# Kernel optimization log

Measured on AMD Instinct MI355X. Metric: run time of the kernel, lower is better.

Reference implementation:

```python
import jax, jax.numpy as jnp
import numpy as np

B, F_C, F_F = 2, 32768, 131072
C_IN, C_OUT, W_DIM, COLOR = 128, 64, 512, 3
K2 = 9
PAD0, PAD1 = 192, 384
ACT_GAIN = float(np.sqrt(2.0))  # lrelu def_gain


def _gather(x, nbr, is_pad, pad):
    # x: [N, C]; nbr: [M, k] indices into [N + pad]; is_pad: [M, k] bool
    padded = jnp.concatenate([x, jnp.zeros((pad, x.shape[1]), x.dtype)], 0)
    g = padded[nbr]  # [M, k, C]
    return jnp.where(is_pad[..., None], jnp.zeros((), x.dtype), g)


def _affine(w, aw, ab):
    # StyleGAN FullyConnectedLayer: runtime weight gain 1/sqrt(fan_in), bias_init=1
    return w @ (aw.T * (1.0 / np.sqrt(aw.shape[1]))) + ab


def _modconv(xg, weight, styles, demodulate=True):
    # xg: [N, k, I]; weight: [O, I, 1, k]; styles: [B, I]
    n, k, ci = xg.shape
    w = weight[:, :, 0, :][None, :, :, :] * styles[:, None, :, None]  # [B,O,I,k]
    if demodulate:
        w = w * jax.lax.rsqrt(jnp.sum(w * w, axis=(2, 3), keepdims=True) + 1e-8)
    xb = xg.reshape(styles.shape[0], -1, k, ci)  # [B,F,k,I]
    return jnp.einsum('bfki,boik->bfo', xb, w).reshape(n, -1)


def _smooth_upsample(x, nbr, is_pad, pad, pool_map):
    # upsample coarse->fine via parent map, then masked neighborhood mean
    xf = x[pool_map]  # [N_fine, C]
    g = _gather(xf, nbr, is_pad, pad)  # [N_fine, k, C]
    cnt = jnp.maximum(jnp.sum(~is_pad, axis=1), 1).astype(x.dtype)
    return jnp.sum(g, axis=1) / cnt[:, None]


def _act(x, gain):
    # clamp_gain(lrelu(x), act_gain*gain, 256*gain)
    y = jnp.where(x >= 0, x, 0.2 * x)
    return jnp.clip(y * (ACT_GAIN * gain), -256.0 * gain, 256.0 * gain)


def setup_inputs():
    key = jax.random.key(0)
    ks = jax.random.split(key, 16)
    x = jax.random.normal(ks[0], (B * F_C, C_IN), jnp.float32)
    img = jax.random.normal(ks[1], (B * F_C, COLOR), jnp.float32)
    ws = jax.random.normal(ks[2], (B, 3, W_DIM), jnp.float32)
    fn0 = jax.random.randint(ks[3], (B * F_C, K2), 0, B * F_C + PAD0, jnp.int32)
    fn1 = jax.random.randint(ks[4], (B * F_F, K2), 0, B * F_F + PAD1, jnp.int32)
    fip0 = jax.random.bernoulli(ks[5], 0.05, (B * F_C, K2))
    fip1 = jax.random.bernoulli(ks[6], 0.05, (B * F_F, K2))
    pool_map0 = jax.random.randint(ks[7], (B * F_F,), 0, B * F_C, jnp.int32)
    a0_w = jax.random.normal(ks[8], (C_IN, W_DIM), jnp.float32)
    a0_b = jnp.ones((C_IN,), jnp.float32)
    W0 = jax.random.normal(ks[9], (C_OUT, C_IN, 1, K2), jnp.float32)
    b0 = jnp.zeros((C_OUT,), jnp.float32)
    ns0 = jnp.zeros((1,), jnp.float32)
    nc0 = jax.random.normal(ks[10], (F_F,), jnp.float32)
    a1_w = jax.random.normal(ks[11], (C_OUT, W_DIM), jnp.float32)
    a1_b = jnp.ones((C_OUT,), jnp.float32)
    W1 = jax.random.normal(ks[12], (C_OUT, C_OUT, 1, K2), jnp.float32)
    b1 = jnp.zeros((C_OUT,), jnp.float32)
    ns1 = jnp.zeros((1,), jnp.float32)
    nc1 = jax.random.normal(ks[13], (F_F,), jnp.float32)
    at_w = jax.random.normal(ks[14], (C_OUT, W_DIM), jnp.float32)
    at_b = jnp.ones((C_OUT,), jnp.float32)
    Wt = jax.random.normal(ks[15], (COLOR, C_OUT, 1, 1), jnp.float32)
    bt = jnp.zeros((COLOR,), jnp.float32)
    return {"x": x, "img": img, "ws": ws, "a0_w": a0_w, "a0_b": a0_b, "W0": W0,
            "b0": b0, "ns0": ns0, "nc0": nc0, "a1_w": a1_w, "a1_b": a1_b,
            "W1": W1, "b1": b1, "ns1": ns1, "nc1": nc1, "at_w": at_w,
            "at_b": at_b, "Wt": Wt, "bt": bt, "fn0": fn0, "fip0": fip0,
            "fn1": fn1, "fip1": fip1, "pool_map0": pool_map0,
            "pad0": PAD0, "pad1": PAD1}


def reference(x, img, ws, a0_w, a0_b, W0, b0, ns0, nc0, a1_w, a1_b, W1, b1, ns1,
              nc1, at_w, at_b, Wt, bt, fn0, fip0, fn1, fip1, pool_map0, pad0, pad1):
    b = ws.shape[0]
    w0, w1, w2 = ws[:, 0], ws[:, 1], ws[:, 2]
    # conv0: coarse gather -> mod conv -> smooth upsample to fine -> noise/bias/act
    s0 = _affine(w0, a0_w, a0_b)
    noise0 = jnp.tile(nc0[None, :], (b, 1)).reshape(-1, 1) * ns0  # noise_mode='const'
    h = _modconv(_gather(x, fn0, fip0, pad0), W0, s0)
    h = _smooth_upsample(h, fn1, fip1, pad1, pool_map0)
    h = _act(h + noise0 + b0[None, :], 1.0)
    # conv1: fine level, no resampler
    s1 = _affine(w1, a1_w, a1_b)
    noise1 = jnp.tile(nc1[None, :], (b, 1)).reshape(-1, 1) * ns1
    h = _modconv(_gather(h, fn1, fip1, pad1), W1, s1)
    h = _act(h + noise1 + b1[None, :], 1.0)
    # torgb: kernel_size=1 -> self index only, no demodulation
    st = _affine(w2, at_w, at_b) * (1.0 / np.sqrt(C_OUT))
    y = _modconv(_gather(h, fn1[:, :1], fip1[:, :1], pad1), Wt, st, demodulate=False)
    y = jnp.clip(y + bt[None, :], -256.0, 256.0)
    img = _smooth_upsample(img, fn1, fip1, pad1, pool_map0) + y
    return (h, img)
```

## Files before the change

### kernel.cpp

```cpp
#include <hip/hip_runtime.h>
#include <hip/hip_bf16.h>

constexpr int F_C   = 32768;
constexpr int F_F   = 131072;
constexpr int N0    = 65536;
constexpr int N1    = 262144;
constexpr int C_IN  = 128;
constexpr int W_DIM = 512;
constexpr int K2c   = 9;
constexpr float RS512     = 0.04419417382415922f;
constexpr float ACT_GAINc = 1.4142135623730951f;

constexpr size_t FO_S0  = 0;
constexpr size_t FO_S1  = 256;
constexpr size_t FO_ST  = 384;
constexpr size_t OFF_WM0T = 2048;
constexpr size_t OFF_WM1T = OFF_WM0T + 294912;
constexpr size_t OFF_H0   = 458752;
constexpr size_t OFF_HA   = OFF_H0 + (size_t)8388608;
constexpr size_t OFF_YPRE = OFF_H0;

typedef short s16x4 __attribute__((ext_vector_type(4)));
typedef float f32x4 __attribute__((ext_vector_type(4)));

__device__ __forceinline__ float b2f(unsigned short u) {
    union { unsigned int i; float f; } v; v.i = ((unsigned int)u) << 16; return v.f;
}
__device__ __forceinline__ unsigned short f2b(float f) {
    __hip_bfloat16 h = __float2bfloat16(f);
    return *reinterpret_cast<unsigned short*>(&h);
}
__device__ __forceinline__ float waveRedSum(float v) {
    for (int m = 32; m; m >>= 1) v += __shfl_xor(v, m, 64);
    return v;
}
__device__ __forceinline__ float actf(float v) {
    float y = (v >= 0.f) ? v : 0.2f * v;
    y *= ACT_GAINc;
    return fminf(fmaxf(y, -256.f), 256.f);
}

__global__ __launch_bounds__(64)
void k_styles(const float* __restrict__ wsF,
              const float* __restrict__ a0w, const float* __restrict__ a0b,
              const float* __restrict__ a1w, const float* __restrict__ a1b,
              const float* __restrict__ atw, const float* __restrict__ atb,
              float* __restrict__ fr)
{
    int bid = blockIdx.x, lane = threadIdx.x;
    int bb, ii, ll, row; const float *aw, *ab; float* dst; float post = 1.f;
    if (bid < 256)      { bb = bid >> 7;             ii = bid & 127; ll = 0; aw = a0w; ab = a0b; dst = fr + FO_S0; row = 128; }
    else if (bid < 384) { int t = bid - 256; bb = t >> 6; ii = t & 63; ll = 1; aw = a1w; ab = a1b; dst = fr + FO_S1; row = 64; }
    else                { int t = bid - 384; bb = t >> 6; ii = t & 63; ll = 2; aw = atw; ab = atb; dst = fr + FO_ST; row = 64; post = 0.125f; }
    const float* wsv = wsF + (size_t)(bb * 3 + ll) * W_DIM;
    const float* awr = aw + (size_t)ii * W_DIM;
    float s = 0.f;
    for (int j = lane; j < W_DIM; j += 64) s += wsv[j] * awr[j];
    s = waveRedSum(s);
    if (lane == 0) dst[bb * row + ii] = (s * RS512 + ab[ii]) * post;
}

__global__ __launch_bounds__(256)
void k_wmod(const float* __restrict__ W0,
            const float* __restrict__ W1,
            const float* __restrict__ fr,
            unsigned short* __restrict__ wm0T,
            unsigned short* __restrict__ wm1T)
{
    int bo = blockIdx.x, tid = threadIdx.x;
    int b, o, CI, NE; const float* W; const float* S; unsigned short* dst;
    if (bo < 128) { b = bo >> 6; o = bo & 63; CI = 128; NE = 1152; W = W0; S = fr + FO_S0; dst = wm0T; }
    else { int t = bo - 128; b = t >> 6; o = t & 63; CI = 64; NE = 576; W = W1; S = fr + FO_S1; dst = wm1T; }
    const float* Wo = W + (size_t)o * NE;
    const float* Sb = S + (size_t)b * CI;
    float ss = 0.f;
    for (int idx = tid; idx < NE; idx += 256) {
        int i = idx / K2c;
        float p = Wo[idx] * Sb[i];
        ss += p * p;
    }
    __shared__ float red[4];
    float s = waveRedSum(ss);
    if ((tid & 63) == 0) red[tid >> 6] = s;
    __syncthreads();
    float d = rsqrtf(red[0] + red[1] + red[2] + red[3] + 1e-8f);
    for (int idx = tid; idx < NE; idx += 256) {
        int i = idx / K2c, kk = idx - i * K2c;
        dst[((size_t)(b * K2c + kk) * 64 + o) * CI + i] = f2b(Wo[idx] * Sb[i] * d);
    }
}

__global__ __launch_bounds__(256)
void k_layer0(const float* __restrict__ xF,
              const int*  __restrict__ fn0,
              const int*  __restrict__ fip0,
              const unsigned short* __restrict__ wm0T,
              unsigned short* __restrict__ h0B)
{
    __shared__ unsigned short A_lds[64 * 136];
    __shared__ unsigned short W_lds[64 * 136];
    __shared__ int snbr[64];
    const int tid  = threadIdx.x;
    const int g0   = blockIdx.x * 64;
    const int b    = g0 / F_C;
    const int wave = tid >> 6, lane = tid & 63;
    const int lg   = lane >> 4, lr = lane & 15;
    f32x4 acc[4] = {};
    for (int kk = 0; kk < K2c; ++kk) {
        __syncthreads();
        if (tid < 64) {
            int g   = g0 + tid;
            int nbr = fn0[(size_t)g * K2c + kk];
            int pd  = fip0[(size_t)g * K2c + kk];
            snbr[tid] = (!pd && nbr < N0) ? nbr : -1;
        }
        __syncthreads();
        {
            int node = tid >> 2, seg = tid & 3;
            int nbr  = snbr[node];
            unsigned short tmp[32];
            if (nbr >= 0) {
                const float4* src = (const float4*)(xF + (size_t)nbr * C_IN + seg * 32);
                #pragma unroll
                for (int q = 0; q < 8; ++q) {
                    float4 f = src[q];
                    tmp[q*4+0] = f2b(f.x); tmp[q*4+1] = f2b(f.y);
                    tmp[q*4+2] = f2b(f.z); tmp[q*4+3] = f2b(f.w);
                }
            } else {
                #pragma unroll
                for (int q = 0; q < 32; ++q) tmp[q] = 0;
            }
            uint4* dstA = (uint4*)(A_lds + node * 136 + seg * 32);
            #pragma unroll
            for (int q = 0; q < 4; ++q) dstA[q] = ((const uint4*)tmp)[q];
            const uint4* wsrc = (const uint4*)(wm0T + ((size_t)(b * K2c + kk) * 64 + node) * C_IN + seg * 32);
            uint4* dstW = (uint4*)(W_lds + node * 136 + seg * 32);
            #pragma unroll
            for (int q = 0; q < 4; ++q) dstW[q] = wsrc[q];
        }
        __syncthreads();
        #pragma unroll
        for (int ks = 0; ks < 8; ++ks) {
            int kb = ks * 16 + lg * 4;
            s16x4 af = *(const s16x4*)(A_lds + (wave * 16 + lr) * 136 + kb);
            #pragma unroll
            for (int nt = 0; nt < 4; ++nt) {
                s16x4 bf = *(const s16x4*)(W_lds + (nt * 16 + lr) * 136 + kb);
                acc[nt] = __builtin_amdgcn_mfma_f32_16x16x16bf16_1k(af, bf, acc[nt], 0, 0, 0);
            }
        }
    }
    #pragma unroll
    for (int nt = 0; nt < 4; ++nt) {
        int o = nt * 16 + lr;
        #pragma unroll
        for (int r = 0; r < 4; ++r) {
            int node = g0 + wave * 16 + lg * 4 + r;
            h0B[(size_t)node * 64 + o] = f2b(acc[nt][r]);
        }
    }
}

__global__ __launch_bounds__(256)
void k_ha(const unsigned short* __restrict__ h0B,
          const int*  __restrict__ fn1,
          const int*  __restrict__ fip1,
          const int*  __restrict__ pool,
          const float* __restrict__ nc0,
          const float* __restrict__ ns0,
          const float* __restrict__ b0,
          unsigned short* __restrict__ haB)
{
    __shared__ int   pmArr[288];
    __shared__ int   vArr[288];
    __shared__ float invCnt[32];
    const int tid = threadIdx.x;
    const int n0  = blockIdx.x * 32;
    for (int idx = tid; idx < 288; idx += 256) {
        int fn = fn1[(size_t)n0 * K2c + idx];
        int ip = fip1[(size_t)n0 * K2c + idx];
        int v  = !ip;
        int pm = -1;
        if (v && fn < N1) pm = pool[fn];
        pmArr[idx] = pm;
        vArr[idx]  = v;
    }
    __syncthreads();
    if (tid < 32) {
        int c = 0;
        #pragma unroll
        for (int k = 0; k < K2c; ++k) c += vArr[tid * K2c + k];
        invCnt[tid] = 1.f / (float)(c > 0 ? c : 1);
    }
    __syncthreads();
    const int wave = tid >> 6, lane = tid & 63;
    const float nsc  = ns0[0];
    const float bias = b0[lane];
    for (int jj = 0; jj < 8; ++jj) {
        int node = wave * 8 + jj;
        int g    = n0 + node;
        float acc = 0.f;
        #pragma unroll
        for (int k = 0; k < K2c; ++k) {
            int pm = pmArr[node * K2c + k];
            int pc = pm >= 0 ? pm : 0;
            float val = b2f(h0B[(size_t)pc * 64 + lane]);
            acc += (pm >= 0) ? val : 0.f;
        }
        float hu = acc * invCnt[node];
        float v  = hu + nc0[g & (F_F - 1)] * nsc + bias;
        haB[(size_t)g * 64 + lane] = f2b(actf(v));
    }
}

__global__ __launch_bounds__(256)
void k_layer1(const unsigned short* __restrict__ haB,
              const int*  __restrict__ fn1,
              const int*  __restrict__ fip1,
              const unsigned short* __restrict__ wm1T,
              const float* __restrict__ nc1,
              const float* __restrict__ ns1,
              const float* __restrict__ b1,
              const float* __restrict__ stS,
              const float* __restrict__ WtF,
              float* __restrict__ hOut,
              float* __restrict__ yPre2)
{
    __shared__ unsigned short A_lds[64 * 72];
    __shared__ unsigned short W_lds[64 * 72];
    __shared__ int snbr[64];
    const int tid  = threadIdx.x;
    const int g0   = blockIdx.x * 64;
    const int b    = g0 / F_F;
    const int wave = tid >> 6, lane = tid & 63;
    const int lg   = lane >> 4, lr = lane & 15;
    f32x4 acc[4] = {};
    for (int kk = 0; kk < K2c; ++kk) {
        __syncthreads();
        if (tid < 64) {
            int g   = g0 + tid;
            int nbr = fn1[(size_t)g * K2c + kk];
            int pd  = fip1[(size_t)g * K2c + kk];
            snbr[tid] = (!pd && nbr < N1) ? nbr : -1;
        }
        __syncthreads();
        {
            int node = tid >> 2, seg = tid & 3;
            int nbr  = snbr[node];
            uint4 v0 = {0,0,0,0}, v1 = {0,0,0,0};
            if (nbr >= 0) {
                const uint4* src = (const uint4*)(haB + (size_t)nbr * 64 + seg * 16);
                v0 = src[0]; v1 = src[1];
            }
            uint4* dstA = (uint4*)(A_lds + node * 72 + seg * 16);
            dstA[0] = v0; dstA[1] = v1;
            const uint4* wsrc = (const uint4*)(wm1T + ((size_t)(b * K2c + kk) * 64 + node) * 64 + seg * 16);
            uint4* dstW = (uint4*)(W_lds + node * 72 + seg * 16);
            dstW[0] = wsrc[0]; dstW[1] = wsrc[1];
        }
        __syncthreads();
        #pragma unroll
        for (int ks = 0; ks < 4; ++ks) {
            int kb = ks * 16 + lg * 4;
            s16x4 af = *(const s16x4*)(A_lds + (wave * 16 + lr) * 72 + kb);
            #pragma unroll
            for (int nt = 0; nt < 4; ++nt) {
                s16x4 bf = *(const s16x4*)(W_lds + (nt * 16 + lr) * 72 + kb);
                acc[nt] = __builtin_amdgcn_mfma_f32_16x16x16bf16_1k(af, bf, acc[nt], 0, 0, 0);
            }
        }
    }
    float nsc = ns1[0];
    float p00[4] = {}, p01[4] = {}, p02[4] = {};
    float p10[4] = {}, p11[4] = {}, p12[4] = {};
    #pragma unroll
    for (int nt = 0; nt < 4; ++nt) {
        int o = nt * 16 + lr;
        float bias = b1[o];
        float st0  = stS[o], st1 = stS[64 + o];
        float wt0 = WtF[o], wt1 = WtF[64 + o], wt2 = WtF[128 + o];
        float w00 = wt0 * st0, w01 = wt1 * st0, w02 = wt2 * st0;
        float w10 = wt0 * st1, w11 = wt1 * st1, w12 = wt2 * st1;
        #pragma unroll
        for (int r = 0; r < 4; ++r) {
            int node = g0 + wave * 16 + lg * 4 + r;
            float v  = actf(acc[nt][r] + nc1[node & (F_F - 1)] * nsc + bias);
            hOut[(size_t)node * 64 + o] = v;
            p00[r] += v * w00; p01[r] += v * w01; p02[r] += v * w02;
            p10[r] += v * w10; p11[r] += v * w11; p12[r] += v * w12;
        }
    }
    #pragma unroll
    for (int m = 1; m < 16; m <<= 1) {
        #pragma unroll
        for (int r = 0; r < 4; ++r) {
            p00[r] += __shfl_xor(p00[r], m, 64);
            p01[r] += __shfl_xor(p01[r], m, 64);
            p02[r] += __shfl_xor(p02[r], m, 64);
            p10[r] += __shfl_xor(p10[r], m, 64);
            p11[r] += __shfl_xor(p11[r], m, 64);
            p12[r] += __shfl_xor(p12[r], m, 64);
        }
    }
    if (lr == 0) {
        #pragma unroll
        for (int r = 0; r < 4; ++r) {
            int node = g0 + wave * 16 + lg * 4 + r;
            yPre2[(size_t)node * 6 + 0] = p00[r];
            yPre2[(size_t)node * 6 + 1] = p01[r];
            yPre2[(size_t)node * 6 + 2] = p02[r];
            yPre2[(size_t)node * 6 + 3] = p10[r];
            yPre2[(size_t)node * 6 + 4] = p11[r];
            yPre2[(size_t)node * 6 + 5] = p12[r];
        }
    }
}

__global__ __launch_bounds__(256)
void k_rgb(const float* __restrict__ yPre2,
           const float* __restrict__ imgF,
           const int*  __restrict__ fn1,
           const int*  __restrict__ fip1,
           const int*  __restrict__ pool,
           const float* __restrict__ btF,
           float* __restrict__ outImg)
{
    const int n = blockIdx.x * 256 + threadIdx.x;
    const int bOut = n / F_F;
    int fn[K2c], ip[K2c];
    #pragma unroll
    for (int k = 0; k < K2c; ++k) {
        fn[k] = fn1[(size_t)n * K2c + k];
        ip[k] = fip1[(size_t)n * K2c + k];
    }
    int pm[K2c], cnt = 0;
    #pragma unroll
    for (int k = 0; k < K2c; ++k) {
        int v  = !ip[k];
        cnt   += v;
        pm[k]  = (v && fn[k] < N1) ? pool[fn[k]] : -1;
    }
    float sr = 0.f, sg = 0.f, sb = 0.f;
    #pragma unroll
    for (int k = 0; k < K2c; ++k) {
        int   pc = pm[k] >= 0 ? pm[k] : 0;
        float m  = pm[k] >= 0 ? 1.f : 0.f;
        sr += m * imgF[(size_t)pc * 3 + 0];
        sg += m * imgF[(size_t)pc * 3 + 1];
        sb += m * imgF[(size_t)pc * 3 + 2];
    }
    int nb0 = (!ip[0] && fn[0] < N1) ? fn[0] : -1;
    float y0 = 0.f, y1 = 0.f, y2 = 0.f;
    if (nb0 >= 0) {
        const float* yp = yPre2 + (size_t)nb0 * 6 + bOut * 3;
        y0 = yp[0]; y1 = yp[1]; y2 = yp[2];
    }
    float ic = 1.f / (float)(cnt > 0 ? cnt : 1);
    y0 = fminf(fmaxf(y0 + btF[0], -256.f), 256.f);
    y1 = fminf(fmaxf(y1 + btF[1], -256.f), 256.f);
    y2 = fminf(fmaxf(y2 + btF[2], -256.f), 256.f);
    outImg[(size_t)n * 3 + 0] = sr * ic + y0;
    outImg[(size_t)n * 3 + 1] = sg * ic + y1;
    outImg[(size_t)n * 3 + 2] = sb * ic + y2;
}

extern "C" void kernel_launch(void* const* d_in, const int* in_sizes, int n_in,
                              void* d_out, int out_size, void* d_ws, size_t ws_size,
                              hipStream_t stream)
{
    const float* xF   = (const float*)d_in[0];
    const float* imgF = (const float*)d_in[1];
    const float* wsF  = (const float*)d_in[2];
    const float* a0w  = (const float*)d_in[3];
    const float* a0b  = (const float*)d_in[4];
    const float* W0w  = (const float*)d_in[5];
    const float* b0w  = (const float*)d_in[6];
    const float* ns0  = (const float*)d_in[7];
    const float* nc0  = (const float*)d_in[8];
    const float* a1w  = (const float*)d_in[9];
    const float* a1b  = (const float*)d_in[10];
    const float* W1w  = (const float*)d_in[11];
    const float* b1w  = (const float*)d_in[12];
    const float* ns1  = (const float*)d_in[13];
    const float* nc1  = (const float*)d_in[14];
    const float* atw  = (const float*)d_in[15];
    const float* atb  = (const float*)d_in[16];
    const float* WtF  = (const float*)d_in[17];
    const float* btF  = (const float*)d_in[18];
    const int* fn0  = (const int*)d_in[19];
    const int* fip0 = (const int*)d_in[20];
    const int* fn1  = (const int*)d_in[21];
    const int* fip1 = (const int*)d_in[22];
    const int* pool = (const int*)d_in[23];

    char* wsb = (char*)d_ws;
    float* fr = (float*)wsb;
    unsigned short* wm0T = (unsigned short*)(wsb + OFF_WM0T);
    unsigned short* wm1T = (unsigned short*)(wsb + OFF_WM1T);
    unsigned short* h0B  = (unsigned short*)(wsb + OFF_H0);
    unsigned short* haB  = (unsigned short*)(wsb + OFF_HA);
    float* yPre2         = (float*)(wsb + OFF_YPRE);

    float* hOut   = (float*)d_out;
    float* imgOut = hOut + (size_t)N1 * 64;

    hipLaunchKernelGGL(k_styles, dim3(512), dim3(64), 0, stream,
                       wsF, a0w, a0b, a1w, a1b, atw, atb, fr);
    hipLaunchKernelGGL(k_wmod, dim3(256), dim3(256), 0, stream,
                       W0w, W1w, fr, wm0T, wm1T);
    hipLaunchKernelGGL(k_layer0, dim3(N0 / 64), dim3(256), 0, stream,
                       xF, fn0, fip0, wm0T, h0B);
    hipLaunchKernelGGL(k_ha, dim3(N1 / 32), dim3(256), 0, stream,
                       h0B, fn1, fip1, pool, nc0, ns0, b0w, haB);
    hipLaunchKernelGGL(k_layer1, dim3(N1 / 64), dim3(256), 0, stream,
                       haB, fn1, fip1, wm1T, nc1, ns1, b1w,
                       fr + FO_ST, WtF, hOut, yPre2);
    hipLaunchKernelGGL(k_rgb, dim3(N1 / 256), dim3(256), 0, stream,
                       yPre2, imgF, fn1, fip1, pool, btF, imgOut);
}
```

Baseline: 219.1 us.

## Use 16x16x32 bf16 MFMA and restructure layer1 gather with register A-fragments and double-buffered weights

Both conv kernels switch from the 16x16x16 bf16 MFMA to the 16x16x32 variant, which halves the instruction count per K-chunk. In k_layer1, all 9 neighbor indices are preloaded into LDS once per block. Each lane then loads its A fragment directly from global memory into registers instead of staging it through LDS. The per-tap weights are double-buffered in LDS so the next tap's load overlaps the current MFMAs, which cuts barriers from three per tap to one. The trade-off is uncoalesced per-lane global gathers and higher register pressure from the nine unrolled taps.

```diff
diff --git a/kernel.cpp b/kernel.cpp
--- a/kernel.cpp
+++ b/kernel.cpp
@@ -20,7 +20,7 @@
 constexpr size_t OFF_HA   = OFF_H0 + (size_t)8388608;
 constexpr size_t OFF_YPRE = OFF_H0;
 
-typedef short s16x4 __attribute__((ext_vector_type(4)));
+typedef short s16x8 __attribute__((ext_vector_type(8)));
 typedef float f32x4 __attribute__((ext_vector_type(4)));
 
 __device__ __forceinline__ float b2f(unsigned short u) {
@@ -141,13 +141,13 @@
         }
         __syncthreads();
         #pragma unroll
-        for (int ks = 0; ks < 8; ++ks) {
-            int kb = ks * 16 + lg * 4;
-            s16x4 af = *(const s16x4*)(A_lds + (wave * 16 + lr) * 136 + kb);
+        for (int ks = 0; ks < 4; ++ks) {
+            int kb = ks * 32 + lg * 8;
+            s16x8 af = *(const s16x8*)(A_lds + (wave * 16 + lr) * 136 + kb);
             #pragma unroll
             for (int nt = 0; nt < 4; ++nt) {
-                s16x4 bf = *(const s16x4*)(W_lds + (nt * 16 + lr) * 136 + kb);
-                acc[nt] = __builtin_amdgcn_mfma_f32_16x16x16bf16_1k(af, bf, acc[nt], 0, 0, 0);
+                s16x8 bf = *(const s16x8*)(W_lds + (nt * 16 + lr) * 136 + kb);
+                acc[nt] = __builtin_amdgcn_mfma_f32_16x16x32_bf16(af, bf, acc[nt], 0, 0, 0);
             }
         }
     }
@@ -227,50 +227,67 @@
               float* __restrict__ hOut,
               float* __restrict__ yPre2)
 {
-    __shared__ unsigned short A_lds[64 * 72];
-    __shared__ unsigned short W_lds[64 * 72];
-    __shared__ int snbr[64];
+    __shared__ unsigned short W_lds[2][64 * 72];
+    __shared__ int snbr[576];
     const int tid  = threadIdx.x;
     const int g0   = blockIdx.x * 64;
     const int b    = g0 / F_F;
     const int wave = tid >> 6, lane = tid & 63;
     const int lg   = lane >> 4, lr = lane & 15;
+
+    const unsigned short* wtap = wm1T + (size_t)b * K2c * 64 * 64;
+
+    for (int idx = tid; idx < 576; idx += 256) {
+        int fn = fn1[(size_t)g0 * K2c + idx];
+        int ip = fip1[(size_t)g0 * K2c + idx];
+        snbr[idx] = (!ip && fn < N1) ? fn : -1;
+    }
+    {
+        const uint4* src = (const uint4*)wtap;
+        int s0 = tid * 2, s1 = s0 + 1;
+        uint4 v0 = src[s0], v1 = src[s1];
+        *(uint4*)(&W_lds[0][(s0 >> 3) * 72 + (s0 & 7) * 8]) = v0;
+        *(uint4*)(&W_lds[0][(s1 >> 3) * 72 + (s1 & 7) * 8]) = v1;
+    }
+    __syncthreads();
+
+    const int row = wave * 16 + lr;
+    int nbrk[9];
+    #pragma unroll
+    for (int k = 0; k < 9; ++k) nbrk[k] = snbr[row * 9 + k];
+
     f32x4 acc[4] = {};
-    for (int kk = 0; kk < K2c; ++kk) {
+    #pragma unroll
+    for (int kk = 0; kk < 9; ++kk) {
+        const int cur = kk & 1;
+        int nbr = nbrk[kk];
+        int pc  = nbr >= 0 ? nbr : 0;
+        const uint4* ap = (const uint4*)(haB + (size_t)pc * 64) + lg;
+        uint4 a0 = ap[0];
+        uint4 a1 = ap[4];
+        if (nbr < 0) { a0 = uint4{0,0,0,0}; a1 = uint4{0,0,0,0}; }
+        if (kk < 8) {
+            const uint4* src = (const uint4*)(wtap + (size_t)(kk + 1) * 4096);
+            int s0 = tid * 2, s1 = s0 + 1;
+            uint4 v0 = src[s0], v1 = src[s1];
+            *(uint4*)(&W_lds[cur ^ 1][(s0 >> 3) * 72 + (s0 & 7) * 8]) = v0;
+            *(uint4*)(&W_lds[cur ^ 1][(s1 >> 3) * 72 + (s1 & 7) * 8]) = v1;
+        }
+        s16x8 af0 = *reinterpret_cast<const s16x8*>(&a0);
+        s16x8 af1 = *reinterpret_cast<const s16x8*>(&a1);
+        #pragma unroll
+        for (int nt = 0; nt < 4; ++nt) {
+            s16x8 bf0 = *(const s16x8*)(&W_lds[cur][(nt * 16 + lr) * 72 + lg * 8]);
+            acc[nt] = __builtin_amdgcn_mfma_f32_16x16x32_bf16(af0, bf0, acc[nt], 0, 0, 0);
+        }
+        #pragma unroll
+        for (int nt = 0; nt < 4; ++nt) {
+            s16x8 bf1 = *(const s16x8*)(&W_lds[cur][(nt * 16 + lr) * 72 + 32 + lg * 8]);
+            acc[nt] = __builtin_amdgcn_mfma_f32_16x16x32_bf16(af1, bf1, acc[nt], 0, 0, 0);
+        }
         __syncthreads();
-        if (tid < 64) {
-            int g   = g0 + tid;
-            int nbr = fn1[(size_t)g * K2c + kk];
-            int pd  = fip1[(size_t)g * K2c + kk];
-            snbr[tid] = (!pd && nbr < N1) ? nbr : -1;
-        }
-        __syncthreads();
-        {
-            int node = tid >> 2, seg = tid & 3;
-            int nbr  = snbr[node];
-            uint4 v0 = {0,0,0,0}, v1 = {0,0,0,0};
-            if (nbr >= 0) {
-                const uint4* src = (const uint4*)(haB + (size_t)nbr * 64 + seg * 16);
-                v0 = src[0]; v1 = src[1];
-            }
-            uint4* dstA = (uint4*)(A_lds + node * 72 + seg * 16);
-            dstA[0] = v0; dstA[1] = v1;
-            const uint4* wsrc = (const uint4*)(wm1T + ((size_t)(b * K2c + kk) * 64 + node) * 64 + seg * 16);
-            uint4* dstW = (uint4*)(W_lds + node * 72 + seg * 16);
-            dstW[0] = wsrc[0]; dstW[1] = wsrc[1];
-        }
-        __syncthreads();
-        #pragma unroll
-        for (int ks = 0; ks < 4; ++ks) {
-            int kb = ks * 16 + lg * 4;
-            s16x4 af = *(const s16x4*)(A_lds + (wave * 16 + lr) * 72 + kb);
-            #pragma unroll
-            for (int nt = 0; nt < 4; ++nt) {
-                s16x4 bf = *(const s16x4*)(W_lds + (nt * 16 + lr) * 72 + kb);
-                acc[nt] = __builtin_amdgcn_mfma_f32_16x16x16bf16_1k(af, bf, acc[nt], 0, 0, 0);
-            }
-        }
-    }
+    }
+
     float nsc = ns1[0];
     float p00[4] = {}, p01[4] = {}, p02[4] = {};
     float p10[4] = {}, p11[4] = {}, p12[4] = {};
```

New measurement: 201.3 us. -8.1%, faster.
